# Performance work log

Hardware: AMD Instinct MI355X
Metric: run time of the kernel (lower is better)

## Reference

```python
import jax, jax.numpy as jnp
import numpy as np

B, C, COUT, L, K = 16, 64, 64, 16384, 3
STRIDE, PAD, DIL, G, DG = 1, 1, 1, 1, 1
LOUT = (L + 2 * PAD - DIL * (K - 1) - 1) // STRIDE + 1


def _conv1d(x, w, b, pad, groups):
    # x: [B, Cin, L], w: [Cout, Cin/groups, k] (torch Conv1d layout)
    y = jax.lax.conv_general_dilated(
        x, w, window_strides=(1,), padding=[(pad, pad)],
        dimension_numbers=('NCH', 'OIH', 'NCH'), feature_group_count=groups)
    return y + b[None, :, None]


def setup_inputs() -> dict:
    key = jax.random.key(0)
    k = jax.random.split(key, 11)
    s = jnp.float32(0.02)  # module init: normal(0, 0.02)
    return {
        'x': jax.random.normal(k[0], (B, C, L), jnp.float32),
        'w_off_dw': jax.random.normal(k[1], (C, 1, 7), jnp.float32) * s,
        'b_off_dw': jax.random.normal(k[2], (C,), jnp.float32) * s,
        'w_off_pw': jax.random.normal(k[3], (G * DG * K, C, 1), jnp.float32) * s,
        'b_off_pw': jax.random.normal(k[4], (G * DG * K,), jnp.float32) * s,
        'w_msk_dw': jax.random.normal(k[5], (C, 1, 7), jnp.float32) * s,
        'b_msk_dw': jax.random.normal(k[6], (C,), jnp.float32) * s,
        'w_msk_pw': jax.random.normal(k[7], (G * DG * K, C, 1), jnp.float32) * s,
        'b_msk_pw': jax.random.normal(k[8], (G * DG * K,), jnp.float32) * s,
        'weight': jax.random.normal(k[9], (COUT, C // G, K), jnp.float32) * s,
        'bias': jax.random.normal(k[10], (COUT,), jnp.float32) * s,
    }


def _deform_conv1d(x, w_off_dw, b_off_dw, w_off_pw, b_off_pw,
                   w_msk_dw, b_msk_dw, w_msk_pw, b_msk_pw, weight, bias):
    # offset / modulation-mask branches: depthwise k=7 conv -> 1x1 conv
    offset = _conv1d(_conv1d(x, w_off_dw, b_off_dw, 3, C), w_off_pw, b_off_pw, 0, 1)  # [B, G*DG*K, Lout]
    mask = jax.nn.sigmoid(_conv1d(_conv1d(x, w_msk_dw, b_msk_dw, 3, C), w_msk_pw, b_msk_pw, 0, 1))

    cpd = C // (G * DG)  # channels per deformable group
    off = jnp.repeat(offset.reshape(B, G * DG, K, LOUT), cpd, axis=1)  # [B, C, K, Lout]
    msk = jnp.repeat(mask.reshape(B, G * DG, K, LOUT), cpd, axis=1)

    base = jnp.arange(LOUT, dtype=x.dtype) * STRIDE - PAD  # [Lout]
    kpos = jnp.arange(K, dtype=x.dtype) * DIL              # [K]
    p = base[None, :] + kpos[:, None]                       # [K, Lout]
    p = p[None, None] + off                                 # fractional sample positions [B, C, K, Lout]

    i0 = jnp.floor(p)
    frac = p - i0
    i0i = i0.astype(jnp.int32)
    i1i = i0i + 1

    xb = jnp.broadcast_to(x[:, :, None, :], (B, C, K, L))
    x0 = jnp.take_along_axis(xb, jnp.clip(i0i, 0, L - 1), axis=-1)
    x1 = jnp.take_along_axis(xb, jnp.clip(i1i, 0, L - 1), axis=-1)
    v0 = ((i0i >= 0) & (i0i < L)).astype(x.dtype)  # zero padding outside
    v1 = ((i1i >= 0) & (i1i < L)).astype(x.dtype)

    # linear interpolation + mask modulation
    val = ((1.0 - frac) * x0 * v0 + frac * x1 * v1) * msk  # [B, C, K, Lout]

    # grouped contraction over (in-channels-per-group, kernel taps)
    out = jnp.einsum('bgikl,goik->bgol',
                     val.reshape(B, G, C // G, K, LOUT),
                     weight.reshape(G, COUT // G, C // G, K))
    return out.reshape(B, COUT, LOUT) + bias[None, :, None]


def reference(x, w_off_dw, b_off_dw, w_off_pw, b_off_pw,
              w_msk_dw, b_msk_dw, w_msk_pw, b_msk_pw, weight, bias):
    return _deform_conv1d(x, w_off_dw, b_off_dw, w_off_pw, b_off_pw,
                          w_msk_dw, b_msk_dw, w_msk_pw, b_msk_pw, weight, bias)
```

## Files before the change

### kernel.cpp

```cpp
#include <hip/hip_runtime.h>
#include <cstdint>

#define LX 16384
#define NB 16
#define LT 64
#define HALO 8
#define XI (LT + 2*HALO)
#define XPD 36

typedef __attribute__((ext_vector_type(2))) _Float16 h2;
typedef __attribute__((ext_vector_type(8))) _Float16 h8;
typedef __attribute__((ext_vector_type(4))) unsigned u4;
typedef __attribute__((ext_vector_type(4))) float f4;

static __device__ __forceinline__ h2 u2h(unsigned u) {
    union { unsigned u; h2 h; } v; v.u = u; return v.h;
}
static __device__ __forceinline__ unsigned h2u(h2 h) {
    union { h2 h; unsigned u; } v; v.h = h; return v.u;
}
static __device__ __forceinline__ unsigned pkrtz(float a, float b) {
    auto r = __builtin_amdgcn_cvt_pkrtz(a, b);
    union { decltype(r) h; unsigned u; } v; v.h = r;
    return v.u;
}

__global__ void prep_kernel(const float* __restrict__ weight,
                            const float* __restrict__ b_off_pw, const float* __restrict__ w_off_pw,
                            const float* __restrict__ b_off_dw,
                            const float* __restrict__ b_msk_pw, const float* __restrict__ w_msk_pw,
                            const float* __restrict__ b_msk_dw,
                            const float* __restrict__ w_off_dw, const float* __restrict__ w_msk_dw,
                            short* __restrict__ A2, float* __restrict__ beff,
                            unsigned* __restrict__ dwt2, unsigned* __restrict__ pwt2) {
    int bid = blockIdx.x;
    int t = threadIdx.x;
    if (bid < 48) {
        int idx = bid * 256 + t;
        int o = idx / 192;
        int rem = idx - o * 192;
        int tap = rem >> 6, c = rem & 63;
        union { _Float16 h; short s; } v;
        v.h = (_Float16)weight[o * 192 + c * 3 + tap];
        A2[idx] = v.s;
    } else {
        for (int idx = t; idx < 448; idx += 256) {
            int br = idx / 224, r2 = idx - br * 224;
            int j = r2 >> 5, cp = r2 & 31;
            const float* src = br ? w_msk_dw : w_off_dw;
            h2 h; h[0] = (_Float16)src[(2 * cp) * 7 + j]; h[1] = (_Float16)src[(2 * cp + 1) * 7 + j];
            dwt2[idx] = h2u(h);
        }
        if (t < 192) {
            int br = t / 96, r2 = t - br * 96;
            int m = r2 >> 5, cp = r2 & 31;
            const float* src = br ? w_msk_pw : w_off_pw;
            h2 h; h[0] = (_Float16)src[m * 64 + 2 * cp]; h[1] = (_Float16)src[m * 64 + 2 * cp + 1];
            pwt2[t] = h2u(h);
        }
        if (t < 6) {
            int br = t / 3, m = t % 3;
            const float* pw = br ? w_msk_pw : w_off_pw;
            const float* bd = br ? b_msk_dw : b_off_dw;
            const float* bp = br ? b_msk_pw : b_off_pw;
            float s = bp[m];
            for (int c = 0; c < 64; ++c) s += pw[m * 64 + c] * bd[c];
            beff[t] = s;
        }
    }
}

__launch_bounds__(256, 4)
__global__ void deform_main(const float* __restrict__ x,
                            const float* __restrict__ bias,
                            const short* __restrict__ A2,
                            const float* __restrict__ beff,
                            const unsigned* __restrict__ dwt2_g,
                            const unsigned* __restrict__ pwt2_g,
                            float* __restrict__ out) {
    __shared__ __align__(16) unsigned xdw[XI * XPD];
    __shared__ __align__(16) unsigned A2l[6144];
    __shared__ __align__(16) unsigned dwt2[448];
    __shared__ __align__(16) unsigned pwt2[192];
    __shared__ unsigned kl_wp[3][64];
    __shared__ int      kl_li[3][64];
    __shared__ float bias_l[64];
    __shared__ float beff_l[8];

    const int t = threadIdx.x;
    const int l0 = blockIdx.x * LT;
    const int b = blockIdx.y;

    const float* xb = x + (size_t)b * (64 * LX);
    #pragma unroll
    for (int s = 0; s < 3; ++s) {
        int p = t + 256 * s;
        if (p < 640) {
            int cp = p & 31, up = p >> 5;
            int g4 = l0 - HALO + up * 4;
            f4 v0 = {0.f, 0.f, 0.f, 0.f}, v1 = {0.f, 0.f, 0.f, 0.f};
            if ((unsigned)g4 < (unsigned)LX) {
                v0 = *(const f4*)(xb + (size_t)(2 * cp) * LX + g4);
                v1 = *(const f4*)(xb + (size_t)(2 * cp + 1) * LX + g4);
            }
            #pragma unroll
            for (int d = 0; d < 4; ++d) {
                int i = up * 4 + d;
                int pc = ((cp >> 3) + i) & 3;
                xdw[i * XPD + pc * 8 + (cp & 7)] = pkrtz(v0[d], v1[d]);
            }
        }
    }
    {
        const u4* A2g4 = (const u4*)A2;
        #pragma unroll
        for (int s = 0; s < 6; ++s) {
            int idx = t + 256 * s;
            int row = idx / 24;
            int g = idx - row * 24;
            int pdw = row * 96 + ((g * 4) ^ ((row & 7) << 2));
            *(u4*)&A2l[pdw] = A2g4[idx];
        }
    }
    for (int idx = t; idx < 448; idx += 256) dwt2[idx] = dwt2_g[idx];
    if (t < 192) pwt2[t] = pwt2_g[t];
    if (t < 64) bias_l[t] = bias[t];
    if (t < 6)  beff_l[t] = beff[t];
    __syncthreads();

    {
        const int l = t >> 2, cc = t & 3;
        h2 so2[8], sm2[8];
        #pragma unroll
        for (int m = 0; m < 8; ++m) { so2[m] = (h2)(_Float16)0; sm2[m] = (h2)(_Float16)0; }
        #pragma unroll
        for (int j = 0; j < 7; ++j) {
            int i = l + 5 + j;
            const unsigned* xr = &xdw[i * XPD + (((cc + i) & 3) << 3)];
            u4 xa = *(const u4*)xr;
            u4 xb2 = *(const u4*)(xr + 4);
            const unsigned* wo = &dwt2[j * 32 + cc * 8];
            const unsigned* wm = &dwt2[224 + j * 32 + cc * 8];
            u4 woa = *(const u4*)wo, wob = *(const u4*)(wo + 4);
            u4 wma = *(const u4*)wm, wmb = *(const u4*)(wm + 4);
            #pragma unroll
            for (int m = 0; m < 4; ++m) {
                so2[m]     += u2h(xa[m])  * u2h(woa[m]);
                so2[m + 4] += u2h(xb2[m]) * u2h(wob[m]);
                sm2[m]     += u2h(xa[m])  * u2h(wma[m]);
                sm2[m + 4] += u2h(xb2[m]) * u2h(wmb[m]);
            }
        }
        float po[3] = {0.f, 0.f, 0.f}, pm[3] = {0.f, 0.f, 0.f};
        #pragma unroll
        for (int m3 = 0; m3 < 3; ++m3) {
            const unsigned* p0 = &pwt2[m3 * 32 + cc * 8];
            const unsigned* p1 = &pwt2[96 + m3 * 32 + cc * 8];
            u4 a0 = *(const u4*)p0, a1 = *(const u4*)(p0 + 4);
            u4 b0 = *(const u4*)p1, b1 = *(const u4*)(p1 + 4);
            #pragma unroll
            for (int m = 0; m < 4; ++m) {
                po[m3] = __builtin_amdgcn_fdot2(so2[m],     u2h(a0[m]), po[m3], false);
                po[m3] = __builtin_amdgcn_fdot2(so2[m + 4], u2h(a1[m]), po[m3], false);
                pm[m3] = __builtin_amdgcn_fdot2(sm2[m],     u2h(b0[m]), pm[m3], false);
                pm[m3] = __builtin_amdgcn_fdot2(sm2[m + 4], u2h(b1[m]), pm[m3], false);
            }
        }
        #pragma unroll
        for (int d = 1; d <= 2; d <<= 1) {
            #pragma unroll
            for (int m3 = 0; m3 < 3; ++m3) {
                po[m3] += __shfl_xor(po[m3], d);
                pm[m3] += __shfl_xor(pm[m3], d);
            }
        }
        if (cc < 3) {
            int k = cc;
            float off = (k == 0 ? po[0] : k == 1 ? po[1] : po[2]) + beff_l[k];
            float z   = (k == 0 ? pm[0] : k == 1 ? pm[1] : pm[2]) + beff_l[3 + k];
            float msk = 1.0f / (1.0f + __expf(-z));
            float p = (float)(l0 + l - 1 + k) + off;
            float fl = floorf(p);
            int i0 = (int)fl, i1 = i0 + 1;
            float fr = p - fl;
            int li0 = i0 - l0 + HALO, li1 = li0 + 1;
            float w0 = (((unsigned)i0 < (unsigned)LX) && ((unsigned)li0 < (unsigned)XI)) ? (1.0f - fr) * msk : 0.0f;
            float w1 = (((unsigned)i1 < (unsigned)LX) && ((unsigned)li1 < (unsigned)XI)) ? fr * msk : 0.0f;
            li0 = min(max(li0, 0), XI - 2);
            kl_wp[k][l] = pkrtz(w0, w1);
            kl_li[k][l] = li0;
        }
    }
    __syncthreads();

    {
        const int lane = t & 63;
        const int wv = t >> 6;
        const int r = lane & 15, q = lane >> 4;
        const int lcol = wv * 16 + r;

        h8 bfr[6];
        #pragma unroll
        for (int kk = 0; kk < 6; ++kk) {
            const int tap = kk >> 1;
            unsigned wp = kl_wp[tap][lcol];
            unsigned w00 = __builtin_amdgcn_perm(wp, wp, 0x01000100u);
            unsigned w11 = __builtin_amdgcn_perm(wp, wp, 0x03020302u);
            int li0 = kl_li[tap][lcol];
            int cp0 = (((kk & 1) << 5) + (q << 3)) >> 1;
            int chunkL = cp0 >> 3;
            int o0 = li0 * XPD + ((((chunkL + li0) & 3) << 3) | (cp0 & 7));
            int o1 = (li0 + 1) * XPD + ((((chunkL + li0 + 1) & 3) << 3) | (cp0 & 7));
            u4 r0 = *(const u4*)&xdw[o0];
            u4 r1 = *(const u4*)&xdw[o1];
            u4 xs;
            #pragma unroll
            for (int d = 0; d < 4; ++d)
                xs[d] = h2u(u2h(r0[d]) * u2h(w00) + u2h(r1[d]) * u2h(w11));
            union { u4 u; h8 h; } cvt; cvt.u = xs;
            bfr[kk] = cvt.h;
        }

        #pragma unroll
        for (int mt = 0; mt < 4; ++mt) {
            f4 acc = {0.f, 0.f, 0.f, 0.f};
            const int row = mt * 16 + r;
            const int rowbase = row * 96;
            const int sw = (r & 7) << 2;
            #pragma unroll
            for (int kk = 0; kk < 6; ++kk) {
                union { u4 u; h8 h; } af;
                af.u = *(const u4*)&A2l[rowbase + ((kk * 16 + q * 4) ^ sw)];
                acc = __builtin_amdgcn_mfma_f32_16x16x32_f16(af.h, bfr[kk], acc, 0, 0, 0);
            }
            int ob = mt * 16 + 4 * q;
            float* op = out + ((size_t)b * 64 + ob) * LX + l0 + lcol;
            #pragma unroll
            for (int e = 0; e < 4; ++e)
                op[(size_t)e * LX] = acc[e] + bias_l[ob + e];
        }
    }
}

extern "C" void kernel_launch(void* const* d_in, const int* in_sizes, int n_in,
                              void* d_out, int out_size, void* d_ws, size_t ws_size,
                              hipStream_t stream) {
    const float* x        = (const float*)d_in[0];
    const float* w_off_dw = (const float*)d_in[1];
    const float* b_off_dw = (const float*)d_in[2];
    const float* w_off_pw = (const float*)d_in[3];
    const float* b_off_pw = (const float*)d_in[4];
    const float* w_msk_dw = (const float*)d_in[5];
    const float* b_msk_dw = (const float*)d_in[6];
    const float* w_msk_pw = (const float*)d_in[7];
    const float* b_msk_pw = (const float*)d_in[8];
    const float* weight   = (const float*)d_in[9];
    const float* bias     = (const float*)d_in[10];
    float* out = (float*)d_out;

    short*    A2   = (short*)d_ws;
    float*    beff = (float*)((char*)d_ws + 24576);
    unsigned* dwt2 = (unsigned*)((char*)d_ws + 24608);
    unsigned* pwt2 = (unsigned*)((char*)d_ws + 26400);

    hipLaunchKernelGGL(prep_kernel, dim3(49), dim3(256), 0, stream,
                       weight, b_off_pw, w_off_pw, b_off_dw, b_msk_pw, w_msk_pw, b_msk_dw,
                       w_off_dw, w_msk_dw, A2, beff, dwt2, pwt2);
    hipLaunchKernelGGL(deform_main, dim3(LX / LT, NB), dim3(256), 0, stream,
                       x, bias, A2, beff, dwt2, pwt2, out);
}
```

Baseline: 155.8 us.

## Process four tiles per block with register-prefetched x loads

```diff
diff --git a/kernel.cpp b/kernel.cpp
--- a/kernel.cpp
+++ b/kernel.cpp
@@ -4,6 +4,7 @@
 #define LX 16384
 #define NB 16
 #define LT 64
+#define TPB 4
 #define HALO 8
 #define XI (LT + 2*HALO)
 #define XPD 36
@@ -24,6 +25,13 @@
     union { decltype(r) h; unsigned u; } v; v.h = r;
     return v.u;
 }
+
+#define BAR_LGKM() do { asm volatile("s_waitcnt lgkmcnt(0)" ::: "memory"); \
+                        __builtin_amdgcn_s_barrier();                      \
+                        asm volatile("" ::: "memory"); } while (0)
+#define BAR_RAW()  do { asm volatile("" ::: "memory");                     \
+                        __builtin_amdgcn_s_barrier();                      \
+                        asm volatile("" ::: "memory"); } while (0)
 
 __global__ void prep_kernel(const float* __restrict__ weight,
                             const float* __restrict__ b_off_pw, const float* __restrict__ w_off_pw,
@@ -88,29 +96,45 @@
     __shared__ float beff_l[8];
 
     const int t = threadIdx.x;
-    const int l0 = blockIdx.x * LT;
+    const int lbase = blockIdx.x * (LT * TPB);
     const int b = blockIdx.y;
-
     const float* xb = x + (size_t)b * (64 * LX);
-    #pragma unroll
-    for (int s = 0; s < 3; ++s) {
-        int p = t + 256 * s;
-        if (p < 640) {
-            int cp = p & 31, up = p >> 5;
-            int g4 = l0 - HALO + up * 4;
-            f4 v0 = {0.f, 0.f, 0.f, 0.f}, v1 = {0.f, 0.f, 0.f, 0.f};
-            if ((unsigned)g4 < (unsigned)LX) {
-                v0 = *(const f4*)(xb + (size_t)(2 * cp) * LX + g4);
-                v1 = *(const f4*)(xb + (size_t)(2 * cp + 1) * LX + g4);
-            }
-            #pragma unroll
-            for (int d = 0; d < 4; ++d) {
-                int i = up * 4 + d;
-                int pc = ((cp >> 3) + i) & 3;
-                xdw[i * XPD + pc * 8 + (cp & 7)] = pkrtz(v0[d], v1[d]);
-            }
-        }
-    }
+
+    f4 rx0[3], rx1[3];
+
+    auto issue_x = [&](int l0v) {
+        #pragma unroll
+        for (int s = 0; s < 3; ++s) {
+            int p = t + 256 * s;
+            rx0[s] = (f4){0.f, 0.f, 0.f, 0.f};
+            rx1[s] = (f4){0.f, 0.f, 0.f, 0.f};
+            if (p < 640) {
+                int cp = p & 31, up = p >> 5;
+                int g4 = l0v - HALO + up * 4;
+                if ((unsigned)g4 < (unsigned)LX) {
+                    rx0[s] = *(const f4*)(xb + (size_t)(2 * cp) * LX + g4);
+                    rx1[s] = *(const f4*)(xb + (size_t)(2 * cp + 1) * LX + g4);
+                }
+            }
+        }
+    };
+    auto write_x = [&]() {
+        #pragma unroll
+        for (int s = 0; s < 3; ++s) {
+            int p = t + 256 * s;
+            if (p < 640) {
+                int cp = p & 31, up = p >> 5;
+                #pragma unroll
+                for (int d = 0; d < 4; ++d) {
+                    int i = up * 4 + d;
+                    int pc = ((cp >> 3) + i) & 3;
+                    xdw[i * XPD + pc * 8 + (cp & 7)] = pkrtz(rx0[s][d], rx1[s][d]);
+                }
+            }
+        }
+    };
+
+    issue_x(lbase);
     {
         const u4* A2g4 = (const u4*)A2;
         #pragma unroll
@@ -126,118 +150,132 @@
     if (t < 192) pwt2[t] = pwt2_g[t];
     if (t < 64) bias_l[t] = bias[t];
     if (t < 6)  beff_l[t] = beff[t];
-    __syncthreads();
-
-    {
-        const int l = t >> 2, cc = t & 3;
-        h2 so2[8], sm2[8];
-        #pragma unroll
-        for (int m = 0; m < 8; ++m) { so2[m] = (h2)(_Float16)0; sm2[m] = (h2)(_Float16)0; }
-        #pragma unroll
-        for (int j = 0; j < 7; ++j) {
-            int i = l + 5 + j;
-            const unsigned* xr = &xdw[i * XPD + (((cc + i) & 3) << 3)];
-            u4 xa = *(const u4*)xr;
-            u4 xb2 = *(const u4*)(xr + 4);
-            const unsigned* wo = &dwt2[j * 32 + cc * 8];
-            const unsigned* wm = &dwt2[224 + j * 32 + cc * 8];
-            u4 woa = *(const u4*)wo, wob = *(const u4*)(wo + 4);
-            u4 wma = *(const u4*)wm, wmb = *(const u4*)(wm + 4);
-            #pragma unroll
-            for (int m = 0; m < 4; ++m) {
-                so2[m]     += u2h(xa[m])  * u2h(woa[m]);
-                so2[m + 4] += u2h(xb2[m]) * u2h(wob[m]);
-                sm2[m]     += u2h(xa[m])  * u2h(wma[m]);
-                sm2[m + 4] += u2h(xb2[m]) * u2h(wmb[m]);
-            }
-        }
-        float po[3] = {0.f, 0.f, 0.f}, pm[3] = {0.f, 0.f, 0.f};
-        #pragma unroll
-        for (int m3 = 0; m3 < 3; ++m3) {
-            const unsigned* p0 = &pwt2[m3 * 32 + cc * 8];
-            const unsigned* p1 = &pwt2[96 + m3 * 32 + cc * 8];
-            u4 a0 = *(const u4*)p0, a1 = *(const u4*)(p0 + 4);
-            u4 b0 = *(const u4*)p1, b1 = *(const u4*)(p1 + 4);
-            #pragma unroll
-            for (int m = 0; m < 4; ++m) {
-                po[m3] = __builtin_amdgcn_fdot2(so2[m],     u2h(a0[m]), po[m3], false);
-                po[m3] = __builtin_amdgcn_fdot2(so2[m + 4], u2h(a1[m]), po[m3], false);
-                pm[m3] = __builtin_amdgcn_fdot2(sm2[m],     u2h(b0[m]), pm[m3], false);
-                pm[m3] = __builtin_amdgcn_fdot2(sm2[m + 4], u2h(b1[m]), pm[m3], false);
-            }
-        }
-        #pragma unroll
-        for (int d = 1; d <= 2; d <<= 1) {
+    write_x();
+    issue_x(lbase + LT);
+    BAR_LGKM();
+
+    #pragma unroll
+    for (int tt = 0; tt < TPB; ++tt) {
+        const int l0 = lbase + tt * LT;
+
+        {
+            const int l = t >> 2, cc = t & 3;
+            h2 so2[8], sm2[8];
+            #pragma unroll
+            for (int m = 0; m < 8; ++m) { so2[m] = (h2)(_Float16)0; sm2[m] = (h2)(_Float16)0; }
+            #pragma unroll
+            for (int j = 0; j < 7; ++j) {
+                int i = l + 5 + j;
+                const unsigned* xr = &xdw[i * XPD + (((cc + i) & 3) << 3)];
+                u4 xa = *(const u4*)xr;
+                u4 xb2 = *(const u4*)(xr + 4);
+                const unsigned* wo = &dwt2[j * 32 + cc * 8];
+                const unsigned* wm = &dwt2[224 + j * 32 + cc * 8];
+                u4 woa = *(const u4*)wo, wob = *(const u4*)(wo + 4);
+                u4 wma = *(const u4*)wm, wmb = *(const u4*)(wm + 4);
+                #pragma unroll
+                for (int m = 0; m < 4; ++m) {
+                    so2[m]     += u2h(xa[m])  * u2h(woa[m]);
+                    so2[m + 4] += u2h(xb2[m]) * u2h(wob[m]);
+                    sm2[m]     += u2h(xa[m])  * u2h(wma[m]);
+                    sm2[m + 4] += u2h(xb2[m]) * u2h(wmb[m]);
+                }
+            }
+            float po[3] = {0.f, 0.f, 0.f}, pm[3] = {0.f, 0.f, 0.f};
             #pragma unroll
             for (int m3 = 0; m3 < 3; ++m3) {
-                po[m3] += __shfl_xor(po[m3], d);
-                pm[m3] += __shfl_xor(pm[m3], d);
-            }
-        }
-        if (cc < 3) {
-            int k = cc;
-            float off = (k == 0 ? po[0] : k == 1 ? po[1] : po[2]) + beff_l[k];
-            float z   = (k == 0 ? pm[0] : k == 1 ? pm[1] : pm[2]) + beff_l[3 + k];
-            float msk = 1.0f / (1.0f + __expf(-z));
-            float p = (float)(l0 + l - 1 + k) + off;
-            float fl = floorf(p);
-            int i0 = (int)fl, i1 = i0 + 1;
-            float fr = p - fl;
-            int li0 = i0 - l0 + HALO, li1 = li0 + 1;
-            float w0 = (((unsigned)i0 < (unsigned)LX) && ((unsigned)li0 < (unsigned)XI)) ? (1.0f - fr) * msk : 0.0f;
-            float w1 = (((unsigned)i1 < (unsigned)LX) && ((unsigned)li1 < (unsigned)XI)) ? fr * msk : 0.0f;
-            li0 = min(max(li0, 0), XI - 2);
-            kl_wp[k][l] = pkrtz(w0, w1);
-            kl_li[k][l] = li0;
-        }
-    }
-    __syncthreads();
-
-    {
-        const int lane = t & 63;
-        const int wv = t >> 6;
-        const int r = lane & 15, q = lane >> 4;
-        const int lcol = wv * 16 + r;
-
-        h8 bfr[6];
-        #pragma unroll
-        for (int kk = 0; kk < 6; ++kk) {
-            const int tap = kk >> 1;
-            unsigned wp = kl_wp[tap][lcol];
-            unsigned w00 = __builtin_amdgcn_perm(wp, wp, 0x01000100u);
-            unsigned w11 = __builtin_amdgcn_perm(wp, wp, 0x03020302u);
-            int li0 = kl_li[tap][lcol];
-            int cp0 = (((kk & 1) << 5) + (q << 3)) >> 1;
-            int chunkL = cp0 >> 3;
-            int o0 = li0 * XPD + ((((chunkL + li0) & 3) << 3) | (cp0 & 7));
-            int o1 = (li0 + 1) * XPD + ((((chunkL + li0 + 1) & 3) << 3) | (cp0 & 7));
-            u4 r0 = *(const u4*)&xdw[o0];
-            u4 r1 = *(const u4*)&xdw[o1];
-            u4 xs;
-            #pragma unroll
-            for (int d = 0; d < 4; ++d)
-                xs[d] = h2u(u2h(r0[d]) * u2h(w00) + u2h(r1[d]) * u2h(w11));
-            union { u4 u; h8 h; } cvt; cvt.u = xs;
-            bfr[kk] = cvt.h;
-        }
-
-        #pragma unroll
-        for (int mt = 0; mt < 4; ++mt) {
-            f4 acc = {0.f, 0.f, 0.f, 0.f};
-            const int row = mt * 16 + r;
-            const int rowbase = row * 96;
-            const int sw = (r & 7) << 2;
+                const unsigned* p0 = &pwt2[m3 * 32 + cc * 8];
+                const unsigned* p1 = &pwt2[96 + m3 * 32 + cc * 8];
+                u4 a0 = *(const u4*)p0, a1 = *(const u4*)(p0 + 4);
+                u4 b0 = *(const u4*)p1, b1 = *(const u4*)(p1 + 4);
+                #pragma unroll
+                for (int m = 0; m < 4; ++m) {
+                    po[m3] = __builtin_amdgcn_fdot2(so2[m],     u2h(a0[m]), po[m3], false);
+                    po[m3] = __builtin_amdgcn_fdot2(so2[m + 4], u2h(a1[m]), po[m3], false);
+                    pm[m3] = __builtin_amdgcn_fdot2(sm2[m],     u2h(b0[m]), pm[m3], false);
+                    pm[m3] = __builtin_amdgcn_fdot2(sm2[m + 4], u2h(b1[m]), pm[m3], false);
+                }
+            }
+            #pragma unroll
+            for (int d = 1; d <= 2; d <<= 1) {
+                #pragma unroll
+                for (int m3 = 0; m3 < 3; ++m3) {
+                    po[m3] += __shfl_xor(po[m3], d);
+                    pm[m3] += __shfl_xor(pm[m3], d);
+                }
+            }
+            if (cc < 3) {
+                int k = cc;
+                float off = (k == 0 ? po[0] : k == 1 ? po[1] : po[2]) + beff_l[k];
+                float z   = (k == 0 ? pm[0] : k == 1 ? pm[1] : pm[2]) + beff_l[3 + k];
+                float msk = 1.0f / (1.0f + __expf(-z));
+                float p = (float)(l0 + l - 1 + k) + off;
+                float fl = floorf(p);
+                int i0 = (int)fl, i1 = i0 + 1;
+                float fr = p - fl;
+                int li0 = i0 - l0 + HALO, li1 = li0 + 1;
+                float w0 = (((unsigned)i0 < (unsigned)LX) && ((unsigned)li0 < (unsigned)XI)) ? (1.0f - fr) * msk : 0.0f;
+                float w1 = (((unsigned)i1 < (unsigned)LX) && ((unsigned)li1 < (unsigned)XI)) ? fr * msk : 0.0f;
+                li0 = min(max(li0, 0), XI - 2);
+                kl_wp[k][l] = pkrtz(w0, w1);
+                kl_li[k][l] = li0;
+            }
+        }
+        BAR_LGKM();
+
+        {
+            const int lane = t & 63;
+            const int wv = t >> 6;
+            const int r = lane & 15, q = lane >> 4;
+            const int lcol = wv * 16 + r;
+
+            h8 bfr[6];
             #pragma unroll
             for (int kk = 0; kk < 6; ++kk) {
-                union { u4 u; h8 h; } af;
-                af.u = *(const u4*)&A2l[rowbase + ((kk * 16 + q * 4) ^ sw)];
-                acc = __builtin_amdgcn_mfma_f32_16x16x32_f16(af.h, bfr[kk], acc, 0, 0, 0);
-            }
-            int ob = mt * 16 + 4 * q;
-            float* op = out + ((size_t)b * 64 + ob) * LX + l0 + lcol;
-            #pragma unroll
-            for (int e = 0; e < 4; ++e)
-                op[(size_t)e * LX] = acc[e] + bias_l[ob + e];
+                const int tap = kk >> 1;
+                unsigned wp = kl_wp[tap][lcol];
+                unsigned w00 = __builtin_amdgcn_perm(wp, wp, 0x01000100u);
+                unsigned w11 = __builtin_amdgcn_perm(wp, wp, 0x03020302u);
+                int li0 = kl_li[tap][lcol];
+                int cp0 = (((kk & 1) << 5) + (q << 3)) >> 1;
+                int chunkL = cp0 >> 3;
+                int o0 = li0 * XPD + ((((chunkL + li0) & 3) << 3) | (cp0 & 7));
+                int o1 = (li0 + 1) * XPD + ((((chunkL + li0 + 1) & 3) << 3) | (cp0 & 7));
+                u4 r0 = *(const u4*)&xdw[o0];
+                u4 r1 = *(const u4*)&xdw[o1];
+                u4 xs;
+                #pragma unroll
+                for (int d = 0; d < 4; ++d)
+                    xs[d] = h2u(u2h(r0[d]) * u2h(w00) + u2h(r1[d]) * u2h(w11));
+                union { u4 u; h8 h; } cvt; cvt.u = xs;
+                bfr[kk] = cvt.h;
+            }
+
+            #pragma unroll
+            for (int mt = 0; mt < 4; ++mt) {
+                f4 acc = {0.f, 0.f, 0.f, 0.f};
+                const int row = mt * 16 + r;
+                const int rowbase = row * 96;
+                const int sw = (r & 7) << 2;
+                #pragma unroll
+                for (int kk = 0; kk < 6; ++kk) {
+                    union { u4 u; h8 h; } af;
+                    af.u = *(const u4*)&A2l[rowbase + ((kk * 16 + q * 4) ^ sw)];
+                    acc = __builtin_amdgcn_mfma_f32_16x16x32_f16(af.h, bfr[kk], acc, 0, 0, 0);
+                }
+                int ob = mt * 16 + 4 * q;
+                float* op = out + ((size_t)b * 64 + ob) * LX + l0 + lcol;
+                #pragma unroll
+                for (int e = 0; e < 4; ++e)
+                    op[(size_t)e * LX] = acc[e] + bias_l[ob + e];
+            }
+        }
+
+        if (tt < TPB - 1) {
+            BAR_RAW();
+            write_x();
+            if (tt + 2 < TPB) issue_x(lbase + (tt + 2) * LT);
+            BAR_LGKM();
         }
     }
 }
@@ -266,6 +304,6 @@
     hipLaunchKernelGGL(prep_kernel, dim3(49), dim3(256), 0, stream,
                        weight, b_off_pw, w_off_pw, b_off_dw, b_msk_pw, w_msk_pw, b_msk_dw,
                        w_off_dw, w_msk_dw, A2, beff, dwt2, pwt2);
-    hipLaunchKernelGGL(deform_main, dim3(LX / LT, NB), dim3(256), 0, stream,
+    hipLaunchKernelGGL(deform_main, dim3(LX / (LT * TPB), NB), dim3(256), 0, stream,
                        x, bias, A2, beff, dwt2, pwt2, out);
 }
```

Measured after the change: 154.4 us. No clear change (-0.9%).
